# Optimization experiments

Hardware: AMD Instinct MI355X
Metric: run time of the kernel (lower is better)

## Reference

```python
import jax, jax.numpy as jnp
import numpy as np

CURVS = (-1.0, 0.0, 1.0, -0.5)
N, E, B = 50000, 800000, 128
IN, HID, OUT, GHID = 128, 128, 128, 32
K = len(CURVS)
TAU_MIN, TAU_MAX = 0.05, 10.0
EPS = 1e-15


def _vnorm(x):
    return jnp.maximum(jnp.linalg.norm(x, axis=-1, keepdims=True), EPS)


def tan_k(x, k):
    if k > 0:
        sk = np.sqrt(k)
        return jnp.tan(x * sk) / sk
    if k < 0:
        sk = np.sqrt(-k)
        return jnp.tanh(x * sk) / sk
    return x


def artan_k(x, k):
    if k > 0:
        sk = np.sqrt(k)
        return jnp.arctan(x * sk) / sk
    if k < 0:
        sk = np.sqrt(-k)
        return jnp.arctanh(jnp.clip(x * sk, -1.0 + 1e-7, 1.0 - 1e-7)) / sk
    return x


def project(x, k):
    # clip inside Poincare ball for k<0; identity otherwise (geoopt Stereographic.projx)
    if k < 0:
        maxn = (1.0 - 1e-5) / np.sqrt(-k)
        n = _vnorm(x)
        return jnp.where(n > maxn, x * (maxn / n), x)
    return x


def expmap0(u, k):
    n = _vnorm(u)
    return project(tan_k(n, k) * u / n, k)


def logmap0(y, k):
    n = _vnorm(y)
    return artan_k(n, k) * y / n


def mobius_add(x, y, k):
    x2 = jnp.sum(x * x, -1, keepdims=True)
    y2 = jnp.sum(y * y, -1, keepdims=True)
    xy = jnp.sum(x * y, -1, keepdims=True)
    num = (1.0 - 2.0 * k * xy - k * y2) * x + (1.0 + k * x2) * y
    den = jnp.maximum(1.0 - 2.0 * k * xy + k * k * x2 * y2, 1e-15)
    return project(num / den, k)


def mobius_matvec(W, x, k):
    mx = x @ W.T
    if k == 0:
        return mx
    xn = _vnorm(x)
    mxn = _vnorm(mx)
    res = tan_k(mxn / xn * artan_k(xn, k), k) * mx / mxn
    res = jnp.where(jnp.sum(jnp.abs(mx), -1, keepdims=True) == 0.0, 0.0, res)
    return project(res, k)


def dist(x, y, k):
    return 2.0 * artan_k(_vnorm(mobius_add(-x, y, k)), k)[..., 0]


def setup_inputs():
    key = jax.random.key(0)
    ks = jax.random.split(key, 12)
    x = jax.random.normal(ks[0], (N, IN), jnp.float32)
    edge_index = jax.random.randint(ks[1], (2, E), 0, N)
    batch = jnp.sort(jax.random.randint(ks[2], (N,), 0, B))
    s1 = float(np.sqrt(2.0 / (IN + HID)))
    s2 = float(np.sqrt(2.0 / (HID + OUT)))
    sg1 = float(np.sqrt(2.0 / (IN + GHID)))
    sg2 = float(np.sqrt(2.0 / (GHID + OUT)))
    raw0 = float(np.log(np.expm1(1.0 - TAU_MIN)))
    return {
        "x": x,
        "edge_index": edge_index,
        "batch": batch,
        "expert_w1": jax.random.normal(ks[3], (K, HID, IN), jnp.float32) * s1,
        "expert_b1": jnp.zeros((K, HID), jnp.float32),
        "expert_w2": jax.random.normal(ks[4], (K, OUT, HID), jnp.float32) * s2,
        "expert_b2": jnp.zeros((K, OUT), jnp.float32),
        "gate_w1": jax.random.normal(ks[5], (GHID, IN), jnp.float32) * sg1,
        "gate_b1": jnp.zeros((GHID,), jnp.float32),
        "gate_w2": jax.random.normal(ks[6], (OUT, GHID), jnp.float32) * sg2,
        "gate_b2": jnp.zeros((OUT,), jnp.float32),
        "gate_u": jax.random.normal(ks[7], (K, OUT), jnp.float32) * 0.02,
        "tau_raw": jnp.full((K,), raw0, jnp.float32),
    }


def _graph_norm(edge_index):
    loops = jnp.arange(N)
    row = jnp.concatenate([edge_index[0], loops])
    col = jnp.concatenate([edge_index[1], loops])
    deg = jax.ops.segment_sum(jnp.ones(E + N, jnp.float32), col, num_segments=N)
    dinv = deg ** -0.5  # deg >= 1 due to self loops
    return row, col, dinv[row] * dinv[col]


def _kappa_conv(xm, W, b, row, col, enorm, k):
    h = mobius_matvec(W, xm, k)
    bias_pt = expmap0(b[None, :], k)  # proju at origin is identity
    h = mobius_add(h, bias_pt, k)
    t = logmap0(h, k)  # [N, out]
    agg = jax.ops.segment_sum(enorm[:, None] * t[row], col, num_segments=N)
    return expmap0(agg, k)


def reference(x, edge_index, batch, expert_w1, expert_b1, expert_w2, expert_b2,
              gate_w1, gate_b1, gate_w2, gate_b2, gate_u, tau_raw):
    x = x.astype(jnp.float32)
    row, col, enorm = _graph_norm(edge_index)
    counts = jnp.maximum(
        jax.ops.segment_sum(jnp.ones(N, jnp.float32), batch, num_segments=B), 1.0)[:, None]

    # --- Riemannian experts ---
    embs = []
    for i, kv in enumerate(CURVS):
        xm = expmap0(x, kv)  # manifold init (proju at origin = identity)
        xm = _kappa_conv(xm, expert_w1[i], expert_b1[i], row, col, enorm, kv)
        xm = _kappa_conv(xm, expert_w2[i], expert_b2[i], row, col, enorm, kv)
        z = logmap0(xm, kv)
        embs.append(jax.ops.segment_sum(z, batch, num_segments=B) / counts)
    features = jnp.concatenate(embs, axis=-1)  # [B, K*OUT]

    # --- Euclidean gating encoder (GCN) ---
    def gcn(h, W, b):
        m = (h @ W.T)
        out = jax.ops.segment_sum(enorm[:, None] * m[row], col, num_segments=N) + b
        return jax.nn.relu(out)

    g = gcn(x, gate_w1, gate_b1)
    g = gcn(g, gate_w2, gate_b2)
    hgate = jax.ops.segment_sum(g, batch, num_segments=B) / counts  # [B, OUT]

    # --- Geometric distance gate ---
    tau = jnp.clip(jax.nn.softplus(tau_raw) + TAU_MIN, TAU_MIN, TAU_MAX)
    dists = []
    for i, kv in enumerate(CURVS):
        zk = expmap0(hgate, kv)
        yk = expmap0(gate_u[i][None, :], kv)
        dists.append(dist(zk, yk, kv))
    dists = jnp.stack(dists, axis=-1)  # [B, K]
    weights = jax.nn.softmax(-dists / tau[None, :], axis=-1)

    scaled = features * jnp.repeat(weights, OUT, axis=1)
    return scaled, weights, dists, tau
```

## Files before the change

### kernel.cpp

```cpp
#include <hip/hip_runtime.h>
#include <math.h>

#define NN 50000
#define EE 800000
#define ETOT (EE + NN)
#define BB 128
#define DIM 128
#define GHID 32
#define CHUNK 128
#define NCHUNK ((ETOT + CHUNK - 1) / CHUNK)
#define SCB 196

#define DEGB 3125
#define G1B 782
#define W2HB 512
#define MEGA0B (DEGB + G1B + W2HB + 1 + 8)
#define PLACEB 3321
#define BNB ((NCHUNK + 255) / 256)

typedef _Float16 f16;
typedef _Float16 f16x2 __attribute__((ext_vector_type(2)));
typedef _Float16 f16x4 __attribute__((ext_vector_type(4)));
typedef _Float16 f16x8 __attribute__((ext_vector_type(8)));
typedef float f32x4 __attribute__((ext_vector_type(4)));

struct CurvPack {
  float k[4], sk[4], mx[4], thr2[4];
};

__device__ __forceinline__ float wsum64(float v) {
#pragma unroll
  for (int m = 32; m; m >>= 1) v += __shfl_xor(v, m, 64);
  return v;
}

__device__ __forceinline__ float tan_k_d(float x, float kv, float sk) {
  if (kv > 0.f) return tanf(x * sk) / sk;
  if (kv < 0.f) return tanhf(x * sk) / sk;
  return x;
}

__device__ __forceinline__ float artan_k_d(float x, float kv, float sk) {
  if (kv > 0.f) return atanf(x * sk) / sk;
  if (kv < 0.f) {
    float t = x * sk;
    t = fminf(fmaxf(t, -1.f + 1e-7f), 1.f - 1e-7f);
    return atanhf(t) / sk;
  }
  return x;
}

__device__ __forceinline__ float proj_scale_d(float n, float kv, float maxn) {
  if (kv < 0.f && n > maxn) return maxn / n;
  return 1.f;
}

__global__ __launch_bounds__(256) void k_mega0(
    const int* __restrict__ ei, float* __restrict__ deg, const int* __restrict__ batch,
    int* __restrict__ boff, float* __restrict__ counts, const float* __restrict__ eb1,
    const float* __restrict__ eb2, float* __restrict__ biasb, const float* __restrict__ ew1,
    const float* __restrict__ ew2, f16* __restrict__ whi, f16* __restrict__ wlo,
    const float* __restrict__ x, const float* __restrict__ gw1, float* __restrict__ m1,
    CurvPack cp) {
  __shared__ float smem[64 * 68 + 64 * 36];
  int bx = blockIdx.x;
  int tid = threadIdx.x;

  if (bx < DEGB) {
    int i = bx * 256 + tid;
    if (i < EE) atomicAdd(&deg[ei[EE + i]], 1.0f);
    return;
  }
  bx -= DEGB;

  if (bx < G1B) {
    float(*xT)[68] = (float(*)[68])smem;
    float(*Wt)[36] = (float(*)[36])(smem + 64 * 68);
    int n0 = bx * 64;
    int c = tid & 7, r = tid >> 3;
    float acc[2][4];
#pragma unroll
    for (int i = 0; i < 2; i++)
#pragma unroll
      for (int jj = 0; jj < 4; jj++) acc[i][jj] = 0.f;
    for (int kc = 0; kc < 2; kc++) {
      if (kc) __syncthreads();
#pragma unroll
      for (int it = 0; it < 8; it++) {
        int u = tid + it * 256;
        int j = u >> 6, kd = u & 63;
        Wt[kd][j] = gw1[j * 128 + kc * 64 + kd];
      }
#pragma unroll
      for (int it = 0; it < 4; it++) {
        int u = tid + it * 256;
        int node = u >> 4, c4 = u & 15;
        float4 v = make_float4(0.f, 0.f, 0.f, 0.f);
        if (n0 + node < NN) v = ((const float4*)x)[(size_t)(n0 + node) * 32 + kc * 16 + c4];
        xT[4 * c4 + 0][node] = v.x;
        xT[4 * c4 + 1][node] = v.y;
        xT[4 * c4 + 2][node] = v.z;
        xT[4 * c4 + 3][node] = v.w;
      }
      __syncthreads();
#pragma unroll 8
      for (int kd = 0; kd < 64; kd++) {
        float2 av = *(const float2*)&xT[kd][r * 2];
        float4 bv = *(const float4*)&Wt[kd][c * 4];
        float a[2] = {av.x, av.y};
        float bbv[4] = {bv.x, bv.y, bv.z, bv.w};
#pragma unroll
        for (int i = 0; i < 2; i++)
#pragma unroll
          for (int jj = 0; jj < 4; jj++) acc[i][jj] = fmaf(a[i], bbv[jj], acc[i][jj]);
      }
    }
#pragma unroll
    for (int i = 0; i < 2; i++) {
      int node = n0 + r * 2 + i;
      if (node >= NN) continue;
      ((float4*)m1)[(size_t)node * 8 + c] =
          make_float4(acc[i][0], acc[i][1], acc[i][2], acc[i][3]);
    }
    return;
  }
  bx -= G1B;

  if (bx < W2HB) {
    int i = bx * 256 + tid;
    if (i >= 8 * 16384) return;
    int slot = i >> 14;
    int r = i & 16383;
    int ex = slot >> 1, layer = slot & 1;
    float w = (layer ? ew2 : ew1)[ex * 16384 + r];
    f16 h = (f16)w;
    whi[i] = h;
    wlo[i] = (f16)(w - (float)h);
    return;
  }
  bx -= W2HB;

  if (bx == 0) {
    int b = tid;
    if (b <= 128) {
      int lo = 0, hi = NN;
      while (lo < hi) {
        int mid = (lo + hi) >> 1;
        if (batch[mid] < b) lo = mid + 1; else hi = mid;
      }
      boff[b] = lo;
    }
    __syncthreads();
    if (b < 128) counts[b] = (float)(boff[b + 1] - boff[b]);
    return;
  }
  bx -= 1;

  {
    float* l2 = smem;
    int ex = bx >> 1, layer = bx & 1;
    float kv = cp.k[ex], sk = cp.sk[ex], maxn = cp.mx[ex];
    const float* b = (layer ? eb2 : eb1) + ex * 128;
    float* outb = biasb + bx * 132;
    int j = tid;
    float v = (j < 128) ? b[j] : 0.f;
    float n2 = wsum64(v * v);
    if ((j & 63) == 0) l2[j >> 6] = n2;
    __syncthreads();
    n2 = l2[0] + l2[1];
    float nraw = sqrtf(n2);
    float nnv = fmaxf(nraw, 1e-15f);
    float tk = tan_k_d(nnv, kv, sk);
    float s = tk / nnv;
    float pn = fmaxf(fabsf(tk) * (nraw / nnv), 1e-15f);
    float ps = proj_scale_d(pn, kv, maxn);
    float bp = ps * s * v;
    if (j < 128) outb[j] = bp;
    float y2v = wsum64(bp * bp);
    __syncthreads();
    if ((j & 63) == 0) l2[j >> 6] = y2v;
    __syncthreads();
    if (j == 0) outb[128] = l2[0] + l2[1];
  }
}

__global__ void k_dinv(float* __restrict__ deg, int* __restrict__ ideg, int n) {
  int i = blockIdx.x * 256 + threadIdx.x;
  if (i < n) {
    float d = deg[i] + 1.0f;
    ideg[i] = (int)(d + 0.5f);
    deg[i] = 1.0f / sqrtf(d);
  }
}

__global__ void k_scanA(const int* __restrict__ ideg, int* __restrict__ bsum, int n) {
  __shared__ int ls[4];
  int i = blockIdx.x * 256 + threadIdx.x;
  int v = (i < n) ? ideg[i] : 0;
#pragma unroll
  for (int m = 1; m < 64; m <<= 1) v += __shfl_xor(v, m, 64);
  if ((threadIdx.x & 63) == 0) ls[threadIdx.x >> 6] = v;
  __syncthreads();
  if (threadIdx.x == 0) bsum[blockIdx.x] = ls[0] + ls[1] + ls[2] + ls[3];
}

__global__ void k_scanB(int* __restrict__ bsum, int nb) {
  __shared__ int wsh[4];
  int tid = threadIdx.x;
  int lane = tid & 63, w = tid >> 6;
  int v = (tid < nb) ? bsum[tid] : 0;
  int x = v;
#pragma unroll
  for (int o = 1; o < 64; o <<= 1) {
    int t = __shfl_up(x, o, 64);
    if (lane >= o) x += t;
  }
  if (lane == 63) wsh[w] = x;
  __syncthreads();
  int add = 0;
  for (int k2 = 0; k2 < w; k2++) add += wsh[k2];
  if (tid < nb) bsum[tid] = add + x - v;
}

__global__ void k_scanC(const int* __restrict__ ideg, const int* __restrict__ bsum,
                        int* __restrict__ off, int* __restrict__ cursor, int n) {
  __shared__ int wsh[4];
  int i = blockIdx.x * 256 + threadIdx.x;
  int lane = threadIdx.x & 63, w = threadIdx.x >> 6;
  int v = (i < n) ? ideg[i] : 0;
  int x = v;
#pragma unroll
  for (int o = 1; o < 64; o <<= 1) {
    int t = __shfl_up(x, o, 64);
    if (lane >= o) x += t;
  }
  if (lane == 63) wsh[w] = x;
  __syncthreads();
  int add = bsum[blockIdx.x];
  for (int k2 = 0; k2 < w; k2++) add += wsh[k2];
  int excl = add + x - v;
  if (i < n) {
    off[i] = excl;
    cursor[i] = excl;
  }
  if (i == n - 1) off[n] = excl + v;
}

__global__ void k_megapre(const int* __restrict__ ei, const float* __restrict__ dinv,
                          int* __restrict__ cursor, int2* __restrict__ esw,
                          const int* __restrict__ off, int* __restrict__ bnode,
                          int* __restrict__ bslot) {
  int bx = blockIdx.x;
  if (bx < PLACEB) {
    int i = bx * 256 + threadIdx.x;
    if (i >= ETOT) return;
    int r_, c_;
    if (i < EE) {
      r_ = ei[i];
      c_ = ei[EE + i];
    } else {
      r_ = i - EE;
      c_ = i - EE;
    }
    int p = atomicAdd(&cursor[c_], 1);
    esw[p] = make_int2(r_, __float_as_int(dinv[r_] * dinv[c_]));
    return;
  }
  bx -= PLACEB;
  int g = bx * 256 + threadIdx.x;
  if (g >= NCHUNK) return;
  int e0 = g * CHUNK;
  int lo = 0, hi = NN;
  while (hi - lo > 1) {
    int mid = (lo + hi) >> 1;
    if (off[mid] <= e0) lo = mid; else hi = mid;
  }
  bnode[g] = lo;
  bslot[g] = (off[lo] + CHUNK - 1) / CHUNK;
}

__device__ __forceinline__ bool span_head(const int* bnode, const int* bslot, const int* off,
                                          int g, int& nd) {
  if (bslot[g] != g) return false;
  nd = bnode[g];
  int s = off[nd], e = off[nd + 1];
  return (s / CHUNK) != ((e - 1) / CHUNK);
}

__global__ __launch_bounds__(256) void k_matmfma(
    const float* __restrict__ A, int astr, int aoffPerEx,
    const f16* __restrict__ whiB, const f16* __restrict__ wloB,
    const float* __restrict__ biasB, int layer, f16* __restrict__ tout, int n,
    const int* __restrict__ bnode, const int* __restrict__ bslot,
    const int* __restrict__ off, float* __restrict__ aggc, CurvPack cp) {
  if (blockIdx.y == 4) {
    int g = blockIdx.x * 4 + (threadIdx.x >> 6);
    int lane = threadIdx.x & 63;
    if (g >= NCHUNK) return;
    int nd;
    if (!span_head(bnode, bslot, off, g, nd)) return;
    float2 z = make_float2(0.f, 0.f);
#pragma unroll
    for (int i = 0; i < 5; i++) ((float2*)aggc)[(size_t)g * 320 + i * 64 + lane] = z;
    return;
  }
  __shared__ float red[3][16][4];
  __shared__ float redT[16][4];
  __shared__ float nAs[16], nCs[16], nL[16];
  int ex = blockIdx.y;
  float kv = cp.k[ex], sk = cp.sk[ex], maxn = cp.mx[ex];
  const f16* whi = whiB + (size_t)(ex * 2 + layer) * 16384;
  const f16* wlo = wloB + (size_t)(ex * 2 + layer) * 16384;
  const float* biasb = biasB + (ex * 2 + layer) * 132;

  int tid = threadIdx.x;
  int w = tid >> 6;
  int lane = tid & 63;
  int col = lane & 15;
  int quad = lane >> 4;
  int n0w = blockIdx.x * 16;
  if (n0w >= n) return;

  int anodec = min(n0w + col, n - 1);
  const float* arow = A + (size_t)anodec * astr + ex * aoffPerEx;
  int jt0 = w * 2;

  f32x4 acc[2];
  acc[0] = (f32x4){0.f, 0.f, 0.f, 0.f};
  acc[1] = (f32x4){0.f, 0.f, 0.f, 0.f};
  float a_n2 = 0.f;

#pragma unroll
  for (int kc = 0; kc < 4; kc++) {
    int kb = kc * 32 + quad * 8;
    float4 a0 = *(const float4*)(arow + kb);
    float4 a1 = *(const float4*)(arow + kb + 4);
    float av[8] = {a0.x, a0.y, a0.z, a0.w, a1.x, a1.y, a1.z, a1.w};
    f16x8 Ah, Al;
#pragma unroll
    for (int i = 0; i < 8; i++) {
      a_n2 = fmaf(av[i], av[i], a_n2);
      f16 h = (f16)av[i];
      Ah[i] = h;
      Al[i] = (f16)(av[i] - (float)h);
    }
#pragma unroll
    for (int j2 = 0; j2 < 2; j2++) {
      const f16* bh = whi + (size_t)((jt0 + j2) * 16 + col) * 128 + kb;
      const f16* bl = wlo + (size_t)((jt0 + j2) * 16 + col) * 128 + kb;
      f16x8 Bh = *(const f16x8*)bh;
      f16x8 Bl = *(const f16x8*)bl;
      acc[j2] = __builtin_amdgcn_mfma_f32_16x16x32_f16(Ah, Bh, acc[j2], 0, 0, 0);
      acc[j2] = __builtin_amdgcn_mfma_f32_16x16x32_f16(Ah, Bl, acc[j2], 0, 0, 0);
      acc[j2] = __builtin_amdgcn_mfma_f32_16x16x32_f16(Al, Bh, acc[j2], 0, 0, 0);
    }
  }
  a_n2 += __shfl_xor(a_n2, 16, 64);
  a_n2 += __shfl_xor(a_n2, 32, 64);

  float bpj[2];
  bpj[0] = biasb[jt0 * 16 + col];
  bpj[1] = biasb[(jt0 + 1) * 16 + col];
  float y2 = biasb[128];

#pragma unroll
  for (int r = 0; r < 4; r++) {
    float s0 = 0.f, s1 = 0.f, s2 = 0.f;
#pragma unroll
    for (int j2 = 0; j2 < 2; j2++) {
      float v = acc[j2][r];
      s0 = fmaf(v, v, s0);
      s1 += fabsf(v);
      s2 = fmaf(v, bpj[j2], s2);
    }
#pragma unroll
    for (int m = 1; m < 16; m <<= 1) {
      s0 += __shfl_xor(s0, m, 64);
      s1 += __shfl_xor(s1, m, 64);
      s2 += __shfl_xor(s2, m, 64);
    }
    if (col == 0) {
      red[0][quad * 4 + r][w] = s0;
      red[1][quad * 4 + r][w] = s1;
      red[2][quad * 4 + r][w] = s2;
    }
  }
  __syncthreads();

  if (tid < 16) {
    float nraw0 = sqrtf(a_n2);
    float nnv0 = fmaxf(nraw0, 1e-15f);
    float tk0 = tan_k_d(nnv0, kv, sk);
    float pn0 = fmaxf(fabsf(tk0) * (nraw0 / nnv0), 1e-15f);
    float ps0 = proj_scale_d(pn0, kv, maxn);
    float sc = (tk0 / nnv0) * ps0;
    float xnr = pn0 * ps0;

    float s0f = (red[0][tid][0] + red[0][tid][1] + red[0][tid][2] + red[0][tid][3]) * sc * sc;
    float s1f = (red[1][tid][0] + red[1][tid][1] + red[1][tid][2] + red[1][tid][3]) * fabsf(sc);
    float s2f = (red[2][tid][0] + red[2][tid][1] + red[2][tid][2] + red[2][tid][3]) * sc;
    float xn = fmaxf(xnr, 1e-15f);
    float mxraw = sqrtf(s0f);
    float mxv = fmaxf(mxraw, 1e-15f);
    float ar = artan_k_d(xn, kv, sk);
    float c1 = tan_k_d(mxv / xn * ar, kv, sk);
    float s = (s1f == 0.f) ? 0.f : c1 / mxv;
    float pn = fmaxf(fabsf(c1) * (mxraw / mxv), 1e-15f);
    float ps = (s1f == 0.f) ? 1.f : proj_scale_d(pn, kv, maxn);
    s *= ps;
    float x2 = (s * s) * s0f;
    float xy = s * s2f;
    float Aa = 1.f - 2.f * kv * xy - kv * y2;
    float Cc = 1.f + kv * x2;
    float den = fmaxf(1.f - 2.f * kv * xy + (kv * kv) * x2 * y2, 1e-15f);
    nAs[tid] = Aa * s / den * sc;
    nCs[tid] = Cc / den;
  }
  __syncthreads();

#pragma unroll
  for (int r = 0; r < 4; r++) {
    int idx = quad * 4 + r;
    float Asc = nAs[idx], Cs = nCs[idx];
    float t0 = 0.f;
#pragma unroll
    for (int j2 = 0; j2 < 2; j2++) {
      float v = fmaf(Asc, acc[j2][r], Cs * bpj[j2]);
      t0 = fmaf(v, v, t0);
    }
#pragma unroll
    for (int m = 1; m < 16; m <<= 1) t0 += __shfl_xor(t0, m, 64);
    if (col == 0) redT[idx][w] = t0;
  }
  __syncthreads();

  if (tid < 16) {
    float t0f = redT[tid][0] + redT[tid][1] + redT[tid][2] + redT[tid][3];
    float nraw = sqrtf(t0f);
    float ps2 = proj_scale_d(fmaxf(nraw, 1e-15f), kv, maxn);
    float nh = fmaxf(ps2 * nraw, 1e-15f);
    nL[tid] = artan_k_d(nh, kv, sk) / nh * ps2;
  }
  __syncthreads();

  f16* tp = tout + (size_t)(ex >> 1) * NN * 256;
  int slot = ex & 1;
#pragma unroll
  for (int r = 0; r < 4; r++) {
    int idx = quad * 4 + r;
    int gnode = n0w + idx;
    if (gnode >= n) continue;
    float Asc = nAs[idx], Cs = nCs[idx], L = nL[idx];
    f16* trow = tp + (size_t)gnode * 256;
#pragma unroll
    for (int j2 = 0; j2 < 2; j2++) {
      float v = fmaf(Asc, acc[j2][r], Cs * bpj[j2]);
      int d = (jt0 + j2) * 16 + col;
      trow[(d >> 1) * 4 + slot * 2 + (d & 1)] = (f16)(L * v);
    }
  }
}

template <int MODE, int PASS>
__global__ __launch_bounds__(256) void k_aggF(
    const int2* __restrict__ esw, const int* __restrict__ off,
    const int* __restrict__ bnode, const int* __restrict__ bslot,
    const int* __restrict__ batch, const f16* __restrict__ tbase,
    const float* __restrict__ gsrc, float* __restrict__ agg1, float* __restrict__ aggc,
    float* __restrict__ g1out, float* __restrict__ feats,
    const float* __restrict__ gbias, const float* __restrict__ gw2,
    float* __restrict__ hgate, int etot, CurvPack cp) {
  __shared__ float gw2s[(MODE == 1 && PASS == 0) ? 32 : 1][128];
  if (MODE == 1 && PASS == 0) {
#pragma unroll
    for (int i2 = 0; i2 < 16; i2++) {
      int u = threadIdx.x + i2 * 256;
      gw2s[u >> 7][u & 127] = gw2[(u & 127) * 32 + (u >> 7)];
    }
    __syncthreads();
  }
  const f16x4* t = (const f16x4*)(tbase + (size_t)PASS * NN * 256);
  int gw = blockIdx.x * 4 + (threadIdx.x >> 6);
  int lane = threadIdx.x & 63;
  int e0 = gw * CHUNK;
  if (e0 >= etot) return;
  int e1 = min(e0 + CHUNK, etot);
  int lane31 = lane & 31;
  int bnHead = bnode[gw];
  int slotA = bslot[gw];
  int slotB = ((gw + 1) * CHUNK < etot) ? bslot[gw + 1] : slotA;

  int2 mv0 = esw[min(e0 + lane, etot - 1)];
  int2 mv1 = esw[min(e0 + 64 + lane, etot - 1)];
  int offv = off[min(bnHead + lane, NN)];
  int batchv = 0;
  if (MODE == 1) batchv = batch[min(bnHead + lane, NN - 1)];

  int cur = bnHead;
  int runStart = __builtin_amdgcn_readlane(offv, 0);
  int eend = __builtin_amdgcn_readlane(offv, 1);

  auto nextOff = [&](int c1) -> int {
    int rel = c1 - bnHead;
    if (rel < 64) return __builtin_amdgcn_readlane(offv, rel);
    return off[c1];
  };
  auto curBatch = [&](int c) -> int {
    int rel = c - bnHead;
    if (rel < 64) return __builtin_amdgcn_readlane(batchv, rel);
    return batch[c];
  };

  float ax[2], ay[2], pax[2], pay[2];
#pragma unroll
  for (int e = 0; e < 2; e++) ax[e] = ay[e] = pax[e] = pay[e] = 0.f;
  float gx = 0.f, pgx = 0.f, pgy = 0.f;
  int bcur = (MODE == 1) ? __builtin_amdgcn_readlane(batchv, 0) : 0;
  float bbx = 0.f, bby = 0.f;
  if (PASS == 0) {
    if (MODE == 0) {
      bbx = gbias[lane31];
    } else {
      float2 bb = ((const float2*)gbias)[lane];
      bbx = bb.x;
      bby = bb.y;
    }
  }

  auto flushInterior = [&]() {
#pragma unroll
    for (int e = 0; e < 2; e++) {
      const int ge = PASS * 2 + e;
      if (MODE == 0) {
        ((float2*)agg1)[(size_t)cur * 256 + ge * 64 + lane] = make_float2(ax[e], ay[e]);
      } else {
        float n2 = wsum64(fmaf(ax[e], ax[e], ay[e] * ay[e]));
        if (n2 <= cp.thr2[ge]) {
          pax[e] += ax[e];
          pay[e] += ay[e];
        } else {
          float nraw = sqrtf(n2);
          float nnv = fmaxf(nraw, 1e-15f);
          float tk = tan_k_d(nnv, cp.k[ge], cp.sk[ge]);
          float s = tk / nnv;
          float pn = fmaxf(fabsf(tk) * (nraw / nnv), 1e-15f);
          float ps = proj_scale_d(pn, cp.k[ge], cp.mx[ge]);
          s *= ps;
          float nh = fmaxf(pn * ps, 1e-15f);
          float sc = artan_k_d(nh, cp.k[ge], cp.sk[ge]) / nh * s;
          pax[e] = fmaf(sc, ax[e], pax[e]);
          pay[e] = fmaf(sc, ay[e], pay[e]);
        }
      }
    }
    if (PASS == 0) {
      if (MODE == 0) {
        if (lane < 32) g1out[(size_t)cur * 32 + lane] = fmaxf(gx + bbx, 0.f);
      } else {
        float o0 = 0.f, o1 = 0.f;
#pragma unroll
        for (int k2 = 0; k2 < 32; k2++) {
          float agk = __int_as_float(__builtin_amdgcn_readlane(__float_as_int(gx), k2));
          float2 wv = *(const float2*)&gw2s[k2][lane * 2];
          o0 = fmaf(agk, wv.x, o0);
          o1 = fmaf(agk, wv.y, o1);
        }
        pgx += fmaxf(o0 + bbx, 0.f);
        pgy += fmaxf(o1 + bby, 0.f);
      }
    }
  };
  auto flushBoundary = [&]() {
    int slot = (cur == bnHead) ? slotA : slotB;
    float* dp = aggc + (size_t)slot * 640;
#pragma unroll
    for (int e = 0; e < 2; e++) {
      const int ge = PASS * 2 + e;
      atomicAdd(dp + ge * 128 + lane * 2, ax[e]);
      atomicAdd(dp + ge * 128 + lane * 2 + 1, ay[e]);
    }
    if (PASS == 0) {
      if (lane < 32) atomicAdd(dp + 512 + lane, gx);
    }
  };
  auto flushPool = [&]() {
#pragma unroll
    for (int e = 0; e < 2; e++) {
      const int ge = PASS * 2 + e;
      float* fp = &feats[(size_t)bcur * 512 + ge * 128 + lane * 2];
      atomicAdd(fp, pax[e]);
      atomicAdd(fp + 1, pay[e]);
    }
    if (PASS == 0) {
      float* hp = &hgate[(size_t)bcur * 128 + lane * 2];
      atomicAdd(hp, pgx);
      atomicAdd(hp + 1, pgy);
    }
  };

  f16x4 rv[8];
  float gf[8];

#pragma unroll
  for (int b = 0; b < CHUNK / 8; b++) {
    int jb = e0 + b * 8;
    if (jb < e1) {
      const int2 mvsel = (b < 8) ? mv0 : mv1;
#pragma unroll
      for (int q = 0; q < 8; q++) {
        int s = __builtin_amdgcn_readlane(mvsel.x, (b & 7) * 8 + q);
        rv[q] = t[(size_t)s * 64 + lane];
        if (PASS == 0) gf[q] = gsrc[(size_t)s * 32 + lane31];
      }
#pragma unroll
      for (int q = 0; q < 8; q++) {
        if (jb + q == eend) {
          if (runStart >= e0) flushInterior(); else flushBoundary();
#pragma unroll
          for (int e = 0; e < 2; e++) ax[e] = ay[e] = 0.f;
          gx = 0.f;
          runStart = jb + q;
          cur++;
          eend = nextOff(cur + 1);
          if (MODE == 1) {
            int nbt = curBatch(cur);
            if (nbt != bcur) {
              flushPool();
#pragma unroll
              for (int e = 0; e < 2; e++) pax[e] = pay[e] = 0.f;
              pgx = pgy = 0.f;
              bcur = nbt;
            }
          }
        }
        float w = __int_as_float(__builtin_amdgcn_readlane(mvsel.y, (b & 7) * 8 + q));
#pragma unroll
        for (int e = 0; e < 2; e++) {
          ax[e] = fmaf(w, (float)rv[q][2 * e], ax[e]);
          ay[e] = fmaf(w, (float)rv[q][2 * e + 1], ay[e]);
        }
        if (PASS == 0) gx = fmaf(w, gf[q], gx);
      }
    }
  }
  if (runStart >= e0 && eend <= e1) flushInterior(); else flushBoundary();
  if (MODE == 1) flushPool();
}

__global__ void k_fix1(const int* __restrict__ bnode, const int* __restrict__ bslot,
                       const int* __restrict__ off, const float* __restrict__ aggc,
                       float* __restrict__ agg1, float* __restrict__ g1,
                       const float* __restrict__ gb1, int nchunk) {
  int g = blockIdx.x * 4 + (threadIdx.x >> 6);
  int lane = threadIdx.x & 63;
  if (g >= nchunk) return;
  int nd;
  if (!span_head(bnode, bslot, off, g, nd)) return;
  const float* sp = aggc + (size_t)g * 640;
#pragma unroll
  for (int e = 0; e < 4; e++) {
    float2 v = ((const float2*)sp)[e * 64 + lane];
    ((float2*)agg1)[(size_t)nd * 256 + e * 64 + lane] = v;
  }
  if (lane < 32) g1[(size_t)nd * 32 + lane] = fmaxf(sp[512 + lane] + gb1[lane], 0.f);
}

__global__ void k_fix2(const int* __restrict__ bnode, const int* __restrict__ bslot,
                       const int* __restrict__ off, const float* __restrict__ aggc,
                       const int* __restrict__ batch, float* __restrict__ feats,
                       const float* __restrict__ gb2, const float* __restrict__ gw2,
                       float* __restrict__ hgate, int nchunk, CurvPack cp) {
  int g = blockIdx.x * 4 + (threadIdx.x >> 6);
  int lane = threadIdx.x & 63;
  if (g >= nchunk) return;
  int nd;
  if (!span_head(bnode, bslot, off, g, nd)) return;
  int b = batch[nd];
  const float* sp = aggc + (size_t)g * 640;
#pragma unroll
  for (int e = 0; e < 4; e++) {
    float2 v = ((const float2*)sp)[e * 64 + lane];
    float n2 = wsum64(fmaf(v.x, v.x, v.y * v.y));
    float nraw = sqrtf(n2);
    float nnv = fmaxf(nraw, 1e-15f);
    float tk = tan_k_d(nnv, cp.k[e], cp.sk[e]);
    float s = tk / nnv;
    float pn = fmaxf(fabsf(tk) * (nraw / nnv), 1e-15f);
    float ps = proj_scale_d(pn, cp.k[e], cp.mx[e]);
    s *= ps;
    float nh = fmaxf(pn * ps, 1e-15f);
    float sc = artan_k_d(nh, cp.k[e], cp.sk[e]) / nh * s;
    float* fp = &feats[(size_t)b * 512 + e * 128 + lane * 2];
    atomicAdd(fp, sc * v.x);
    atomicAdd(fp + 1, sc * v.y);
  }
  float2 bb = ((const float2*)gb2)[lane];
  float o0 = 0.f, o1 = 0.f;
#pragma unroll 8
  for (int k2 = 0; k2 < 32; k2++) {
    float agk = sp[512 + k2];
    o0 = fmaf(agk, gw2[(2 * lane) * 32 + k2], o0);
    o1 = fmaf(agk, gw2[(2 * lane + 1) * 32 + k2], o1);
  }
  float* hp = &hgate[(size_t)b * 128 + lane * 2];
  atomicAdd(hp, fmaxf(o0 + bb.x, 0.f));
  atomicAdd(hp + 1, fmaxf(o1 + bb.y, 0.f));
}

__global__ __launch_bounds__(128) void k_final(const float* __restrict__ feats,
                                               const float* __restrict__ hgate,
                                               const float* __restrict__ counts,
                                               const float* __restrict__ gate_u,
                                               const float* __restrict__ tau_raw,
                                               float* __restrict__ out, CurvPack cp) {
  __shared__ float l2[2];
  int b = blockIdx.x;
  int j = threadIdx.x;
  float cnt = fmaxf(counts[b], 1.f);
  float hg = hgate[(size_t)b * 128 + j] / cnt;

  auto bsum = [&](float v) -> float {
    v = wsum64(v);
    __syncthreads();
    if ((j & 63) == 0) l2[j >> 6] = v;
    __syncthreads();
    return l2[0] + l2[1];
  };

  float nhg2 = bsum(hg * hg);
  float nhgraw = sqrtf(nhg2);
  float nhg = fmaxf(nhgraw, 1e-15f);

  float d[4], tau[4];
#pragma unroll
  for (int i = 0; i < 4; i++) {
    float kv = cp.k[i], sk = cp.sk[i], mxn = cp.mx[i];
    float tk = tan_k_d(nhg, kv, sk);
    float s = tk / nhg;
    float pn = fmaxf(fabsf(tk) * (nhgraw / nhg), 1e-15f);
    s *= proj_scale_d(pn, kv, mxn);
    float zk = s * hg;

    float u = gate_u[i * 128 + j];
    float nu2 = bsum(u * u);
    float nuraw = sqrtf(nu2);
    float nu = fmaxf(nuraw, 1e-15f);
    float tku = tan_k_d(nu, kv, sk);
    float su = tku / nu;
    float pnu = fmaxf(fabsf(tku) * (nuraw / nu), 1e-15f);
    su *= proj_scale_d(pnu, kv, mxn);
    float yk = su * u;

    float xv = -zk;
    float x2 = bsum(xv * xv);
    float y2 = bsum(yk * yk);
    float xy = bsum(xv * yk);
    float A = 1.f - 2.f * kv * xy - kv * y2;
    float C = 1.f + kv * x2;
    float den = fmaxf(1.f - 2.f * kv * xy + (kv * kv) * x2 * y2, 1e-15f);
    float ma = (A * xv + C * yk) / den;
    float m2 = bsum(ma * ma);
    float mraw = sqrtf(m2);
    float ps2 = proj_scale_d(fmaxf(mraw, 1e-15f), kv, mxn);
    float nm = fmaxf(ps2 * mraw, 1e-15f);
    d[i] = 2.f * artan_k_d(nm, kv, sk);

    float tr = tau_raw[i];
    tau[i] = fminf(fmaxf(log1pf(expf(tr)) + 0.05f, 0.05f), 10.f);
  }

  float xi[4];
  float mxv = -1e30f;
#pragma unroll
  for (int i = 0; i < 4; i++) {
    xi[i] = -d[i] / tau[i];
    mxv = fmaxf(mxv, xi[i]);
  }
  float es = 0.f, e[4];
#pragma unroll
  for (int i = 0; i < 4; i++) {
    e[i] = expf(xi[i] - mxv);
    es += e[i];
  }
  float w[4];
#pragma unroll
  for (int i = 0; i < 4; i++) w[i] = e[i] / es;

#pragma unroll
  for (int i = 0; i < 4; i++)
    out[(size_t)b * 512 + i * 128 + j] = feats[(size_t)b * 512 + i * 128 + j] / cnt * w[i];

  if (j < 4) {
    out[65536 + b * 4 + j] = w[j];
    out[66048 + b * 4 + j] = d[j];
  }
  if (b == 0 && j < 4) out[66560 + j] = tau[j];
}

extern "C" void kernel_launch(void* const* d_in, const int* in_sizes, int n_in,
                              void* d_out, int out_size, void* d_ws, size_t ws_size,
                              hipStream_t stream) {
  const float* x = (const float*)d_in[0];
  const int* ei = (const int*)d_in[1];
  const int* batch = (const int*)d_in[2];
  const float* ew1 = (const float*)d_in[3];
  const float* eb1 = (const float*)d_in[4];
  const float* ew2 = (const float*)d_in[5];
  const float* eb2 = (const float*)d_in[6];
  const float* gw1 = (const float*)d_in[7];
  const float* gb1 = (const float*)d_in[8];
  const float* gw2 = (const float*)d_in[9];
  const float* gb2 = (const float*)d_in[10];
  const float* gu = (const float*)d_in[11];
  const float* traw = (const float*)d_in[12];
  float* out = (float*)d_out;

  const int N = NN, E = EE, ET = ETOT, B = BB;

  float* ws = (float*)d_ws;
  size_t o = 0;
  f16* t4 = (f16*)ws;       o += (size_t)N * 256;
  float* agg1 = ws + o;     o += (size_t)N * 512;
  float* aggc = ws + o;     o += (size_t)NCHUNK * 640;
  float* deg = ws + o;      o += N;
  float* counts = ws + o;   o += 256;
  float* feats = ws + o;    o += (size_t)B * 512;
  float* hg = ws + o;       o += (size_t)B * 128;
  float* biasb = ws + o;    o += 8 * 132;
  f16* whi = (f16*)(ws + o);    o += 8 * 16384 / 2;
  f16* wlo = (f16*)(ws + o);    o += 8 * 16384 / 2;
  float* m1 = ws + o;       o += (size_t)N * 32;
  float* g1 = ws + o;       o += (size_t)N * 32;
  int* ideg = (int*)(ws + o);   o += N;
  int* csroff = (int*)(ws + o); o += N + 8;
  int* cursor = (int*)(ws + o); o += N;
  int* boff = (int*)(ws + o);   o += 136;
  int* bsum = (int*)(ws + o);   o += 256;
  int* bnode = (int*)(ws + o);  o += NCHUNK + 8;
  int* bslot = (int*)(ws + o);  o += NCHUNK + 8;
  int2* esw = (int2*)(ws + o);  o += (size_t)2 * ET;

  hipMemsetAsync(deg, 0, ((size_t)N + 256 + (size_t)B * 512 + (size_t)B * 128) * sizeof(float),
                 stream);

  const double curvs[4] = {-1.0, 0.0, 1.0, -0.5};
  CurvPack cp;
  for (int i = 0; i < 4; i++) {
    double kd = curvs[i];
    double skd = sqrt(fabs(kd));
    cp.k[i] = (float)kd;
    cp.sk[i] = (float)skd;
    cp.mx[i] = (kd < 0) ? (float)((1.0 - 1e-5) / skd) : 3.0e38f;
    if (kd < 0) {
      double thr = 6.0 / skd;
      cp.thr2[i] = (float)(thr * thr);
    } else if (kd > 0) {
      double thr = 1.5 / skd;
      cp.thr2[i] = (float)(thr * thr);
    } else {
      cp.thr2[i] = 3.0e38f;
    }
  }

  k_mega0<<<MEGA0B, 256, 0, stream>>>(ei, deg, batch, boff, counts, eb1, eb2, biasb, ew1, ew2,
                                      whi, wlo, x, gw1, m1, cp);
  k_dinv<<<SCB, 256, 0, stream>>>(deg, ideg, N);
  k_scanA<<<SCB, 256, 0, stream>>>(ideg, bsum, N);
  k_scanB<<<1, 256, 0, stream>>>(bsum, SCB);
  k_scanC<<<SCB, 256, 0, stream>>>(ideg, bsum, csroff, cursor, N);
  k_megapre<<<PLACEB + BNB, 256, 0, stream>>>(ei, deg, cursor, esw, csroff, bnode, bslot);

  const int aggBlocks = (NCHUNK + 3) / 4;
  dim3 mfmaGrid((N + 15) / 16, 5);

  k_matmfma<<<mfmaGrid, 256, 0, stream>>>(x, 128, 0, whi, wlo, biasb, 0, t4, N, bnode, bslot,
                                          csroff, aggc, cp);
  k_aggF<0, 0><<<aggBlocks, 256, 0, stream>>>(esw, csroff, bnode, bslot, batch, t4, m1, agg1,
                                              aggc, g1, nullptr, gb1, nullptr, nullptr, ET, cp);
  k_aggF<0, 1><<<aggBlocks, 256, 0, stream>>>(esw, csroff, bnode, bslot, batch, t4, nullptr,
                                              agg1, aggc, nullptr, nullptr, nullptr, nullptr,
                                              nullptr, ET, cp);
  k_fix1<<<aggBlocks, 256, 0, stream>>>(bnode, bslot, csroff, aggc, agg1, g1, gb1, NCHUNK);

  k_matmfma<<<mfmaGrid, 256, 0, stream>>>(agg1, 512, 128, whi, wlo, biasb, 1, t4, N, bnode,
                                          bslot, csroff, aggc, cp);
  k_aggF<1, 0><<<aggBlocks, 256, 0, stream>>>(esw, csroff, bnode, bslot, batch, t4, g1, nullptr,
                                              aggc, nullptr, feats, gb2, gw2, hg, ET, cp);
  k_aggF<1, 1><<<aggBlocks, 256, 0, stream>>>(esw, csroff, bnode, bslot, batch, t4, nullptr,
                                              nullptr, aggc, nullptr, feats, nullptr, nullptr,
                                              nullptr, ET, cp);
  k_fix2<<<aggBlocks, 256, 0, stream>>>(bnode, bslot, csroff, aggc, batch, feats, gb2, gw2, hg,
                                        NCHUNK, cp);

  k_final<<<B, 128, 0, stream>>>(feats, hg, counts, gu, traw, out, cp);

  (void)in_sizes; (void)n_in; (void)out_size; (void)ws_size;
}
```

Baseline: 912.6 us.

## Process all four curvature experts per block and stage outputs for coalesced stores

The mobius matvec kernel now handles all four experts for a 16-node tile in a single block, replacing a 2D grid with one expert per block. Results are staged in shared memory and written as full 16-byte rows instead of scattered 2-byte interleaved stores. The aggc-zeroing work moves into extra 1D blocks. Each thread now holds four times the accumulators, which raises register pressure and may reduce occupancy.

```diff
diff --git a/kernel.cpp b/kernel.cpp
--- a/kernel.cpp
+++ b/kernel.cpp
@@ -17,6 +17,8 @@
 #define MEGA0B (DEGB + G1B + W2HB + 1 + 8)
 #define PLACEB 3321
 #define BNB ((NCHUNK + 255) / 256)
+#define NB ((NN + 15) / 16)
+#define ZB ((NCHUNK + 3) / 4)
 
 typedef _Float16 f16;
 typedef _Float16 f16x2 __attribute__((ext_vector_type(2)));
@@ -293,8 +295,8 @@
     const float* __restrict__ biasB, int layer, f16* __restrict__ tout, int n,
     const int* __restrict__ bnode, const int* __restrict__ bslot,
     const int* __restrict__ off, float* __restrict__ aggc, CurvPack cp) {
-  if (blockIdx.y == 4) {
-    int g = blockIdx.x * 4 + (threadIdx.x >> 6);
+  if (blockIdx.x >= NB) {
+    int g = (blockIdx.x - NB) * 4 + (threadIdx.x >> 6);
     int lane = threadIdx.x & 63;
     if (g >= NCHUNK) return;
     int nd;
@@ -304,14 +306,12 @@
     for (int i = 0; i < 5; i++) ((float2*)aggc)[(size_t)g * 320 + i * 64 + lane] = z;
     return;
   }
-  __shared__ float red[3][16][4];
-  __shared__ float redT[16][4];
-  __shared__ float nAs[16], nCs[16], nL[16];
-  int ex = blockIdx.y;
-  float kv = cp.k[ex], sk = cp.sk[ex], maxn = cp.mx[ex];
-  const f16* whi = whiB + (size_t)(ex * 2 + layer) * 16384;
-  const f16* wlo = wloB + (size_t)(ex * 2 + layer) * 16384;
-  const float* biasb = biasB + (ex * 2 + layer) * 132;
+
+  __shared__ float red[3][4][16][4];
+  __shared__ float redT[4][16][4];
+  __shared__ float nAs[4][16], nCs[4][16], nL[4][16];
+  __shared__ float sm_an2[4][16];
+  __shared__ f16 tstage[16][512];
 
   int tid = threadIdx.x;
   int w = tid >> 6;
@@ -319,76 +319,98 @@
   int col = lane & 15;
   int quad = lane >> 4;
   int n0w = blockIdx.x * 16;
-  if (n0w >= n) return;
 
   int anodec = min(n0w + col, n - 1);
-  const float* arow = A + (size_t)anodec * astr + ex * aoffPerEx;
   int jt0 = w * 2;
 
-  f32x4 acc[2];
-  acc[0] = (f32x4){0.f, 0.f, 0.f, 0.f};
-  acc[1] = (f32x4){0.f, 0.f, 0.f, 0.f};
-  float a_n2 = 0.f;
-
-#pragma unroll
-  for (int kc = 0; kc < 4; kc++) {
-    int kb = kc * 32 + quad * 8;
-    float4 a0 = *(const float4*)(arow + kb);
-    float4 a1 = *(const float4*)(arow + kb + 4);
-    float av[8] = {a0.x, a0.y, a0.z, a0.w, a1.x, a1.y, a1.z, a1.w};
-    f16x8 Ah, Al;
-#pragma unroll
-    for (int i = 0; i < 8; i++) {
-      a_n2 = fmaf(av[i], av[i], a_n2);
-      f16 h = (f16)av[i];
-      Ah[i] = h;
-      Al[i] = (f16)(av[i] - (float)h);
-    }
-#pragma unroll
-    for (int j2 = 0; j2 < 2; j2++) {
-      const f16* bh = whi + (size_t)((jt0 + j2) * 16 + col) * 128 + kb;
-      const f16* bl = wlo + (size_t)((jt0 + j2) * 16 + col) * 128 + kb;
-      f16x8 Bh = *(const f16x8*)bh;
-      f16x8 Bl = *(const f16x8*)bl;
-      acc[j2] = __builtin_amdgcn_mfma_f32_16x16x32_f16(Ah, Bh, acc[j2], 0, 0, 0);
-      acc[j2] = __builtin_amdgcn_mfma_f32_16x16x32_f16(Ah, Bl, acc[j2], 0, 0, 0);
-      acc[j2] = __builtin_amdgcn_mfma_f32_16x16x32_f16(Al, Bh, acc[j2], 0, 0, 0);
-    }
-  }
-  a_n2 += __shfl_xor(a_n2, 16, 64);
-  a_n2 += __shfl_xor(a_n2, 32, 64);
-
-  float bpj[2];
-  bpj[0] = biasb[jt0 * 16 + col];
-  bpj[1] = biasb[(jt0 + 1) * 16 + col];
-  float y2 = biasb[128];
-
-#pragma unroll
-  for (int r = 0; r < 4; r++) {
-    float s0 = 0.f, s1 = 0.f, s2 = 0.f;
-#pragma unroll
-    for (int j2 = 0; j2 < 2; j2++) {
-      float v = acc[j2][r];
-      s0 = fmaf(v, v, s0);
-      s1 += fabsf(v);
-      s2 = fmaf(v, bpj[j2], s2);
-    }
-#pragma unroll
-    for (int m = 1; m < 16; m <<= 1) {
-      s0 += __shfl_xor(s0, m, 64);
-      s1 += __shfl_xor(s1, m, 64);
-      s2 += __shfl_xor(s2, m, 64);
-    }
-    if (col == 0) {
-      red[0][quad * 4 + r][w] = s0;
-      red[1][quad * 4 + r][w] = s1;
-      red[2][quad * 4 + r][w] = s2;
+  f32x4 acc[4][2];
+#pragma unroll
+  for (int ex = 0; ex < 4; ex++)
+#pragma unroll
+    for (int j2 = 0; j2 < 2; j2++) acc[ex][j2] = (f32x4){0.f, 0.f, 0.f, 0.f};
+  float a_n2[4];
+
+#pragma unroll
+  for (int ex = 0; ex < 4; ex++) {
+    const float* arow = A + (size_t)anodec * astr + ex * aoffPerEx;
+    const f16* whi = whiB + (size_t)(ex * 2 + layer) * 16384;
+    const f16* wlo = wloB + (size_t)(ex * 2 + layer) * 16384;
+    a_n2[ex] = 0.f;
+#pragma unroll
+    for (int kc = 0; kc < 4; kc++) {
+      int kb = kc * 32 + quad * 8;
+      float4 a0 = *(const float4*)(arow + kb);
+      float4 a1 = *(const float4*)(arow + kb + 4);
+      float av[8] = {a0.x, a0.y, a0.z, a0.w, a1.x, a1.y, a1.z, a1.w};
+      f16x8 Ah, Al;
+#pragma unroll
+      for (int i = 0; i < 8; i++) {
+        a_n2[ex] = fmaf(av[i], av[i], a_n2[ex]);
+        f16 h = (f16)av[i];
+        Ah[i] = h;
+        Al[i] = (f16)(av[i] - (float)h);
+      }
+#pragma unroll
+      for (int j2 = 0; j2 < 2; j2++) {
+        const f16* bh = whi + (size_t)((jt0 + j2) * 16 + col) * 128 + kb;
+        const f16* bl = wlo + (size_t)((jt0 + j2) * 16 + col) * 128 + kb;
+        f16x8 Bh = *(const f16x8*)bh;
+        f16x8 Bl = *(const f16x8*)bl;
+        acc[ex][j2] = __builtin_amdgcn_mfma_f32_16x16x32_f16(Ah, Bh, acc[ex][j2], 0, 0, 0);
+        acc[ex][j2] = __builtin_amdgcn_mfma_f32_16x16x32_f16(Ah, Bl, acc[ex][j2], 0, 0, 0);
+        acc[ex][j2] = __builtin_amdgcn_mfma_f32_16x16x32_f16(Al, Bh, acc[ex][j2], 0, 0, 0);
+      }
+    }
+    a_n2[ex] += __shfl_xor(a_n2[ex], 16, 64);
+    a_n2[ex] += __shfl_xor(a_n2[ex], 32, 64);
+  }
+
+  if (tid < 16) {
+#pragma unroll
+    for (int ex = 0; ex < 4; ex++) sm_an2[ex][tid] = a_n2[ex];
+  }
+
+  float bpj[4][2];
+#pragma unroll
+  for (int ex = 0; ex < 4; ex++) {
+    const float* biasb = biasB + (ex * 2 + layer) * 132;
+    bpj[ex][0] = biasb[jt0 * 16 + col];
+    bpj[ex][1] = biasb[(jt0 + 1) * 16 + col];
+  }
+
+#pragma unroll
+  for (int ex = 0; ex < 4; ex++) {
+#pragma unroll
+    for (int r = 0; r < 4; r++) {
+      float s0 = 0.f, s1 = 0.f, s2 = 0.f;
+#pragma unroll
+      for (int j2 = 0; j2 < 2; j2++) {
+        float v = acc[ex][j2][r];
+        s0 = fmaf(v, v, s0);
+        s1 += fabsf(v);
+        s2 = fmaf(v, bpj[ex][j2], s2);
+      }
+#pragma unroll
+      for (int m = 1; m < 16; m <<= 1) {
+        s0 += __shfl_xor(s0, m, 64);
+        s1 += __shfl_xor(s1, m, 64);
+        s2 += __shfl_xor(s2, m, 64);
+      }
+      if (col == 0) {
+        red[0][ex][quad * 4 + r][w] = s0;
+        red[1][ex][quad * 4 + r][w] = s1;
+        red[2][ex][quad * 4 + r][w] = s2;
+      }
     }
   }
   __syncthreads();
 
-  if (tid < 16) {
-    float nraw0 = sqrtf(a_n2);
+  if (tid < 64) {
+    int nd = tid & 15, ex = tid >> 4;
+    float kv = cp.k[ex], sk = cp.sk[ex], maxn = cp.mx[ex];
+    float y2 = biasB[(ex * 2 + layer) * 132 + 128];
+    float an2 = sm_an2[ex][nd];
+    float nraw0 = sqrtf(an2);
     float nnv0 = fmaxf(nraw0, 1e-15f);
     float tk0 = tan_k_d(nnv0, kv, sk);
     float pn0 = fmaxf(fabsf(tk0) * (nraw0 / nnv0), 1e-15f);
@@ -396,9 +418,12 @@
     float sc = (tk0 / nnv0) * ps0;
     float xnr = pn0 * ps0;
 
-    float s0f = (red[0][tid][0] + red[0][tid][1] + red[0][tid][2] + red[0][tid][3]) * sc * sc;
-    float s1f = (red[1][tid][0] + red[1][tid][1] + red[1][tid][2] + red[1][tid][3]) * fabsf(sc);
-    float s2f = (red[2][tid][0] + red[2][tid][1] + red[2][tid][2] + red[2][tid][3]) * sc;
+    float s0f = (red[0][ex][nd][0] + red[0][ex][nd][1] + red[0][ex][nd][2] + red[0][ex][nd][3]) *
+                sc * sc;
+    float s1f = (red[1][ex][nd][0] + red[1][ex][nd][1] + red[1][ex][nd][2] + red[1][ex][nd][3]) *
+                fabsf(sc);
+    float s2f = (red[2][ex][nd][0] + red[2][ex][nd][1] + red[2][ex][nd][2] + red[2][ex][nd][3]) *
+                sc;
     float xn = fmaxf(xnr, 1e-15f);
     float mxraw = sqrtf(s0f);
     float mxv = fmaxf(mxraw, 1e-15f);
@@ -413,50 +438,70 @@
     float Aa = 1.f - 2.f * kv * xy - kv * y2;
     float Cc = 1.f + kv * x2;
     float den = fmaxf(1.f - 2.f * kv * xy + (kv * kv) * x2 * y2, 1e-15f);
-    nAs[tid] = Aa * s / den * sc;
-    nCs[tid] = Cc / den;
+    nAs[ex][nd] = Aa * s / den * sc;
+    nCs[ex][nd] = Cc / den;
   }
   __syncthreads();
 
 #pragma unroll
-  for (int r = 0; r < 4; r++) {
-    int idx = quad * 4 + r;
-    float Asc = nAs[idx], Cs = nCs[idx];
-    float t0 = 0.f;
-#pragma unroll
-    for (int j2 = 0; j2 < 2; j2++) {
-      float v = fmaf(Asc, acc[j2][r], Cs * bpj[j2]);
-      t0 = fmaf(v, v, t0);
-    }
-#pragma unroll
-    for (int m = 1; m < 16; m <<= 1) t0 += __shfl_xor(t0, m, 64);
-    if (col == 0) redT[idx][w] = t0;
+  for (int ex = 0; ex < 4; ex++) {
+#pragma unroll
+    for (int r = 0; r < 4; r++) {
+      int idx = quad * 4 + r;
+      float Asc = nAs[ex][idx], Cs = nCs[ex][idx];
+      float t0 = 0.f;
+#pragma unroll
+      for (int j2 = 0; j2 < 2; j2++) {
+        float v = fmaf(Asc, acc[ex][j2][r], Cs * bpj[ex][j2]);
+        t0 = fmaf(v, v, t0);
+      }
+#pragma unroll
+      for (int m = 1; m < 16; m <<= 1) t0 += __shfl_xor(t0, m, 64);
+      if (col == 0) redT[ex][idx][w] = t0;
+    }
   }
   __syncthreads();
 
-  if (tid < 16) {
-    float t0f = redT[tid][0] + redT[tid][1] + redT[tid][2] + redT[tid][3];
+  if (tid < 64) {
+    int nd = tid & 15, ex = tid >> 4;
+    float kv = cp.k[ex], sk = cp.sk[ex], maxn = cp.mx[ex];
+    float t0f = redT[ex][nd][0] + redT[ex][nd][1] + redT[ex][nd][2] + redT[ex][nd][3];
     float nraw = sqrtf(t0f);
     float ps2 = proj_scale_d(fmaxf(nraw, 1e-15f), kv, maxn);
     float nh = fmaxf(ps2 * nraw, 1e-15f);
-    nL[tid] = artan_k_d(nh, kv, sk) / nh * ps2;
+    nL[ex][nd] = artan_k_d(nh, kv, sk) / nh * ps2;
   }
   __syncthreads();
 
-  f16* tp = tout + (size_t)(ex >> 1) * NN * 256;
-  int slot = ex & 1;
-#pragma unroll
-  for (int r = 0; r < 4; r++) {
-    int idx = quad * 4 + r;
-    int gnode = n0w + idx;
-    if (gnode >= n) continue;
-    float Asc = nAs[idx], Cs = nCs[idx], L = nL[idx];
-    f16* trow = tp + (size_t)gnode * 256;
-#pragma unroll
-    for (int j2 = 0; j2 < 2; j2++) {
-      float v = fmaf(Asc, acc[j2][r], Cs * bpj[j2]);
-      int d = (jt0 + j2) * 16 + col;
-      trow[(d >> 1) * 4 + slot * 2 + (d & 1)] = (f16)(L * v);
+#pragma unroll
+  for (int ex = 0; ex < 4; ex++) {
+    const int pair = ex >> 1, slot = ex & 1;
+#pragma unroll
+    for (int r = 0; r < 4; r++) {
+      int idx = quad * 4 + r;
+      float Asc = nAs[ex][idx], Cs = nCs[ex][idx], L = nL[ex][idx];
+#pragma unroll
+      for (int j2 = 0; j2 < 2; j2++) {
+        float v = fmaf(Asc, acc[ex][j2][r], Cs * bpj[ex][j2]);
+        int d = (jt0 + j2) * 16 + col;
+        tstage[idx][pair * 256 + (d >> 1) * 4 + slot * 2 + (d & 1)] = (f16)(L * v);
+      }
+    }
+  }
+  __syncthreads();
+
+#pragma unroll
+  for (int p = 0; p < 2; p++) {
+    f16* tp = tout + (size_t)p * NN * 256;
+#pragma unroll
+    for (int it = 0; it < 2; it++) {
+      int u = tid + it * 256;
+      int row = u >> 5;
+      int c8 = u & 31;
+      int gnode = n0w + row;
+      if (gnode < n)
+        *((f16x8*)(tp + (size_t)gnode * 256) + c8) =
+            *((const f16x8*)&tstage[row][p * 256] + c8);
     }
   }
 }
@@ -871,10 +916,10 @@
   k_megapre<<<PLACEB + BNB, 256, 0, stream>>>(ei, deg, cursor, esw, csroff, bnode, bslot);
 
   const int aggBlocks = (NCHUNK + 3) / 4;
-  dim3 mfmaGrid((N + 15) / 16, 5);
-
-  k_matmfma<<<mfmaGrid, 256, 0, stream>>>(x, 128, 0, whi, wlo, biasb, 0, t4, N, bnode, bslot,
-                                          csroff, aggc, cp);
+  const int mfmaBlocks = NB + ZB;
+
+  k_matmfma<<<mfmaBlocks, 256, 0, stream>>>(x, 128, 0, whi, wlo, biasb, 0, t4, N, bnode, bslot,
+                                            csroff, aggc, cp);
   k_aggF<0, 0><<<aggBlocks, 256, 0, stream>>>(esw, csroff, bnode, bslot, batch, t4, m1, agg1,
                                               aggc, g1, nullptr, gb1, nullptr, nullptr, ET, cp);
   k_aggF<0, 1><<<aggBlocks, 256, 0, stream>>>(esw, csroff, bnode, bslot, batch, t4, nullptr,
@@ -882,8 +927,8 @@
                                               nullptr, ET, cp);
   k_fix1<<<aggBlocks, 256, 0, stream>>>(bnode, bslot, csroff, aggc, agg1, g1, gb1, NCHUNK);
 
-  k_matmfma<<<mfmaGrid, 256, 0, stream>>>(agg1, 512, 128, whi, wlo, biasb, 1, t4, N, bnode,
-                                          bslot, csroff, aggc, cp);
+  k_matmfma<<<mfmaBlocks, 256, 0, stream>>>(agg1, 512, 128, whi, wlo, biasb, 1, t4, N, bnode,
+                                            bslot, csroff, aggc, cp);
   k_aggF<1, 0><<<aggBlocks, 256, 0, stream>>>(esw, csroff, bnode, bslot, batch, t4, g1, nullptr,
                                               aggc, nullptr, feats, gb2, gw2, hg, ET, cp);
   k_aggF<1, 1><<<aggBlocks, 256, 0, stream>>>(esw, csroff, bnode, bslot, batch, t4, nullptr,
```

New measurement: 1.012 ms. 10.9% more time.
